# Optimization experiments

Hardware: AMD Instinct MI355X
Metric: run time of the kernel (lower is better)

The kernel has to match this reference:

```python
import jax, jax.numpy as jnp
import numpy as np

N = 10000
F_IN = 512
HID = 256
N_CLS = 64


def setup_inputs() -> dict:
    key = jax.random.key(0)
    k_feat, k_adj, k_w1, k_b1, k_w2, k_b2 = jax.random.split(key, 6)
    feature = jax.random.normal(k_feat, (N, F_IN), dtype=jnp.float32)
    # normalized-adjacency-like dense matrix (sparse-ish values, scaled)
    adj = jax.random.uniform(k_adj, (N, N), dtype=jnp.float32) * (1.0 / N)
    # GCNConv params: glorot-style weights, zero bias
    s1 = 1.0 / np.sqrt(F_IN)
    s2 = 1.0 / np.sqrt(HID)
    W1 = jax.random.uniform(k_w1, (F_IN, HID), jnp.float32, -s1, s1)
    b1 = jnp.zeros((HID,), jnp.float32)
    W2 = jax.random.uniform(k_w2, (HID, N_CLS), jnp.float32, -s2, s2)
    b2 = jnp.zeros((N_CLS,), jnp.float32)
    return {"feature": feature, "adj": adj, "W1": W1, "b1": b1, "W2": W2, "b2": b2}


def gcn_conv(x, adj, W, b):
    # support = x @ W ; out = adj @ support + b
    return adj @ (x @ W) + b


def reference(feature, adj, W1, b1, W2, b2):
    x1 = jax.nn.relu(gcn_conv(feature, adj, W1, b1))
    # dropout is identity in eval mode
    x2 = gcn_conv(x1, adj, W2, b2)
    return (x1, jax.nn.log_softmax(x2, axis=1))
```

## Files before the change

### kernel.cpp

```cpp
#include <hip/hip_runtime.h>
#include <hip/hip_bf16.h>


#define NROW 10000
#define FIN  512
#define HID  256
#define NCLS 64
#define KP   10048
#define KSPLIT2 4
#define KSPAN2  2560
#define KSPLIT4 8
#define KSPAN4  1280

typedef __bf16 bf8_t __attribute__((ext_vector_type(8)));
typedef __bf16 bf4_t __attribute__((ext_vector_type(4)));
typedef float  f4_t  __attribute__((ext_vector_type(4)));

typedef __attribute__((address_space(3))) void       lds_void;
typedef const __attribute__((address_space(1))) void glb_void;

__device__ __forceinline__ void dma16(const void* g, void* l) {
    __builtin_amdgcn_global_load_lds((glb_void*)g, (lds_void*)l, 16, 0, 0);
}

__device__ __forceinline__ int swzc(int k, int r) {
    return (k & ~63) | ((((k >> 3) & 7) ^ (r & 7)) << 3) | (k & 7);
}

template<int LDW>
__global__ void cvt_f32_bf16_swz(const float* __restrict__ in, __bf16* __restrict__ out, int n) {
    int stride = gridDim.x * blockDim.x * 4;
    for (int i = (blockIdx.x * blockDim.x + threadIdx.x) * 4; i < n; i += stride) {
        f4_t v = *(const f4_t*)(in + i);
        bf4_t o;
        o[0] = (__bf16)v[0]; o[1] = (__bf16)v[1]; o[2] = (__bf16)v[2]; o[3] = (__bf16)v[3];
        int row = i / LDW, k = i & (LDW - 1);
        *(bf4_t*)(out + (long)row * LDW + swzc(k, row)) = o;
    }
}

__global__ void cvt_transpose(const float* __restrict__ in, __bf16* __restrict__ out, int K, int Nn) {
    int idx = blockIdx.x * 256 + threadIdx.x;
    if (idx < K * Nn) {
        int k = idx / Nn, n = idx % Nn;
        out[(long)n * K + swzc(k, n)] = (__bf16)in[idx];
    }
}

template<int BN, bool AF32, int EPI>
__global__ void __launch_bounds__(256, (BN >= 128) ? 3 : 4)
gemm_bt(const void* __restrict__ Ap, const __bf16* __restrict__ Bt,
        int M, int Nn, int K, int Kclamp, int lda, int ldb, int kspan,
        float* __restrict__ outF, __bf16* __restrict__ outB,
        int ldo, long partStride)
{
    constexpr int BM = 64, BK = 64;
    constexpr int WM = BM / 2, WN = BN / 2;
    constexpr int MI = WM / 16, NI = WN / 16;
    constexpr int ACALLS = BM / 32;
    constexpr int BCALLS = BN / 32;
    constexpr int ASZ = BM * BK, BSZ = BN * BK;
    __shared__ __bf16 As[2 * ASZ];
    __shared__ __bf16 Bs[2 * BSZ];

    const int tid  = threadIdx.x;
    const int lane = tid & 63;
    const int wave = tid >> 6;
    const int wm = wave >> 1, wn = wave & 1;
    const int m0 = blockIdx.x * BM;
    const int n0 = blockIdx.y * BN;
    const int kbase = blockIdx.z * kspan;
    const int kend  = min(K, kbase + kspan);

    f4_t acc[MI][NI];
    #pragma unroll
    for (int i = 0; i < MI; i++)
        #pragma unroll
        for (int j = 0; j < NI; j++)
            acc[i][j] = f4_t{0.f, 0.f, 0.f, 0.f};

    const int lrow  = lane & 15;
    const int koff0 = (lane >> 4) * 8;
    const int l7    = lrow & 7;

    const __bf16* Brow[BCALLS];
    #pragma unroll
    for (int j = 0; j < BCALLS; ++j) {
        int c = wave + j * 4;
        Brow[j] = Bt + (long)(n0 + c * 8 + (lane >> 3)) * ldb + (lane & 7) * 8;
    }
    const __bf16* ArowB[ACALLS];
    const float*  ArowF[4];
    int Acol[4], AldsOff[4];
    if constexpr (AF32) {
        #pragma unroll
        for (int i = 0; i < 4; ++i) {
            int idx = tid + i * 256;
            int r = idx >> 4, c4 = idx & 15;
            ArowF[i] = (const float*)Ap + (long)min(m0 + r, M - 1) * lda;
            Acol[i] = c4 * 4;
            AldsOff[i] = r * BK + ((((c4 >> 1) ^ (r & 7)) << 3) | ((c4 & 1) * 4));
        }
    } else {
        #pragma unroll
        for (int j = 0; j < ACALLS; ++j) {
            int c = wave + j * 4;
            ArowB[j] = (const __bf16*)Ap + (long)(m0 + c * 8 + (lane >> 3)) * lda + (lane & 7) * 8;
        }
    }

    if constexpr (AF32) {
        f4_t av[4];
        #pragma unroll
        for (int i = 0; i < 4; ++i)
            av[i] = *(const f4_t*)(ArowF[i] + min(kbase + Acol[i], Kclamp - 4));
        #pragma unroll
        for (int i = 0; i < 4; ++i) {
            bf4_t o;
            o[0] = (__bf16)av[i][0]; o[1] = (__bf16)av[i][1];
            o[2] = (__bf16)av[i][2]; o[3] = (__bf16)av[i][3];
            *(bf4_t*)&As[AldsOff[i]] = o;
        }
    } else {
        #pragma unroll
        for (int j = 0; j < ACALLS; ++j)
            dma16(ArowB[j] + kbase, &As[(wave + j * 4) * 512]);
    }
    #pragma unroll
    for (int j = 0; j < BCALLS; ++j)
        dma16(Brow[j] + kbase, &Bs[(wave + j * 4) * 512]);
    __syncthreads();

    int cur = 0;
    for (int k0 = kbase; k0 < kend; k0 += BK) {
        const bool has_next = (k0 + BK < kend);
        const int nxt = cur ^ 1;
        f4_t av[4];
        if (has_next) {
            if constexpr (AF32) {
                #pragma unroll
                for (int i = 0; i < 4; ++i)
                    av[i] = *(const f4_t*)(ArowF[i] + min(k0 + BK + Acol[i], Kclamp - 4));
            } else {
                #pragma unroll
                for (int j = 0; j < ACALLS; ++j)
                    dma16(ArowB[j] + (k0 + BK), &As[nxt * ASZ + (wave + j * 4) * 512]);
            }
            #pragma unroll
            for (int j = 0; j < BCALLS; ++j)
                dma16(Brow[j] + (k0 + BK), &Bs[nxt * BSZ + (wave + j * 4) * 512]);
        }

        #pragma unroll
        for (int ks = 0; ks < BK; ks += 32) {
            const int cc = (ks + koff0) >> 3;
            const int co = ((cc ^ l7) << 3);
            bf8_t af[MI], bfv[NI];
            #pragma unroll
            for (int mi = 0; mi < MI; mi++)
                af[mi] = *(const bf8_t*)&As[cur * ASZ + (wm * WM + mi * 16 + lrow) * BK + co];
            #pragma unroll
            for (int ni = 0; ni < NI; ni++)
                bfv[ni] = *(const bf8_t*)&Bs[cur * BSZ + (wn * WN + ni * 16 + lrow) * BK + co];
            #pragma unroll
            for (int mi = 0; mi < MI; mi++)
                #pragma unroll
                for (int ni = 0; ni < NI; ni++)
                    acc[mi][ni] = __builtin_amdgcn_mfma_f32_16x16x32_bf16(
                        af[mi], bfv[ni], acc[mi][ni], 0, 0, 0);
        }

        if (has_next) {
            if constexpr (AF32) {
                #pragma unroll
                for (int i = 0; i < 4; ++i) {
                    bf4_t o;
                    o[0] = (__bf16)av[i][0]; o[1] = (__bf16)av[i][1];
                    o[2] = (__bf16)av[i][2]; o[3] = (__bf16)av[i][3];
                    *(bf4_t*)&As[nxt * ASZ + AldsOff[i]] = o;
                }
            }
        }
        __syncthreads();
        cur ^= 1;
    }

    const int erow = wm * WM + (lane >> 4) * 4;
    const int ecol = wn * WN + lrow;
    #pragma unroll
    for (int mi = 0; mi < MI; mi++) {
        #pragma unroll
        for (int ni = 0; ni < NI; ni++) {
            #pragma unroll
            for (int r = 0; r < 4; r++) {
                int grow = m0 + erow + mi * 16 + r;
                int gcol = n0 + ecol + ni * 16;
                if (grow < M && gcol < Nn) {
                    float v = acc[mi][ni][r];
                    if constexpr (EPI == 0) {
                        outB[(long)grow * ldo + swzc(gcol, grow)] = (__bf16)v;
                    } else {
                        outF[blockIdx.z * partStride + (long)grow * ldo + gcol] = v;
                    }
                }
            }
        }
    }
}

__global__ void relu_bias_fin(const float* __restrict__ part, const float* __restrict__ b1,
                              float* __restrict__ outF, __bf16* __restrict__ outB) {
    long i = (long)(blockIdx.x * 256 + threadIdx.x) * 4;
    f4_t v = *(const f4_t*)(part + i);
    #pragma unroll
    for (int s = 1; s < KSPLIT2; s++) {
        f4_t p = *(const f4_t*)(part + (long)s * NROW * HID + i);
        v[0] += p[0]; v[1] += p[1]; v[2] += p[2]; v[3] += p[3];
    }
    int row = (int)(i >> 8);
    int col = (int)(i & (HID - 1));
    f4_t b = *(const f4_t*)(b1 + col);
    f4_t y;
    bf4_t yb;
    #pragma unroll
    for (int j = 0; j < 4; j++) {
        y[j] = fmaxf(v[j] + b[j], 0.f);
        yb[j] = (__bf16)y[j];
    }
    *(f4_t*)(outF + i) = y;
    *(bf4_t*)(outB + (long)row * HID + swzc(col, row)) = yb;
}

__global__ void logsoftmax_fin(const float* __restrict__ part, const float* __restrict__ b2,
                               float* __restrict__ out, int M) {
    int row  = blockIdx.x * 4 + (threadIdx.x >> 6);
    int lane = threadIdx.x & 63;
    if (row >= M) return;
    float v = b2[lane];
    #pragma unroll
    for (int s = 0; s < KSPLIT4; s++) v += part[((long)s * M + row) * NCLS + lane];
    float m = v;
    #pragma unroll
    for (int off = 32; off > 0; off >>= 1) m = fmaxf(m, __shfl_xor(m, off));
    float e = __expf(v - m);
    float sum = e;
    #pragma unroll
    for (int off = 32; off > 0; off >>= 1) sum += __shfl_xor(sum, off);
    out[(long)row * NCLS + lane] = (v - m) - __logf(sum);
}

extern "C" void kernel_launch(void* const* d_in, const int* in_sizes, int n_in,
                              void* d_out, int out_size, void* d_ws, size_t ws_size,
                              hipStream_t stream) {
    const float* feat = (const float*)d_in[0];
    const float* adj  = (const float*)d_in[1];
    const float* W1   = (const float*)d_in[2];
    const float* b1   = (const float*)d_in[3];
    const float* W2   = (const float*)d_in[4];
    const float* b2   = (const float*)d_in[5];
    float* out = (float*)d_out;
    char* ws = (char*)d_ws;

    __bf16* featb = (__bf16*)(ws);
    __bf16* W1t   = (__bf16*)(ws + 10289152);
    __bf16* W2t   = (__bf16*)(ws + 10551296);
    __bf16* S1t   = (__bf16*)(ws + 10584064);
    __bf16* x1b   = (__bf16*)(ws + 15728640);
    __bf16* S2t   = (__bf16*)(ws + 20873216);
    float*  part  = (float*) (ws + 22159360);

    hipMemsetAsync(S1t, 0, (size_t)HID * KP * 2, stream);
    hipMemsetAsync(S2t, 0, (size_t)NCLS * KP * 2, stream);

    cvt_f32_bf16_swz<FIN><<<640, 256, 0, stream>>>(feat, featb, NROW * FIN);
    cvt_transpose<<<(FIN * HID + 255) / 256, 256, 0, stream>>>(W1, W1t, FIN, HID);
    cvt_transpose<<<(HID * NCLS + 255) / 256, 256, 0, stream>>>(W2, W2t, HID, NCLS);

    gemm_bt<64, false, 0><<<dim3(4, 157, 1), 256, 0, stream>>>(
        W1t, featb, HID, NROW, FIN, FIN, FIN, FIN, FIN,
        nullptr, S1t, KP, 0);

    gemm_bt<128, true, 2><<<dim3(157, 2, KSPLIT2), 256, 0, stream>>>(
        adj, S1t, NROW, HID, KP, NROW, NROW, KP, KSPAN2,
        part, nullptr, HID, (long)NROW * HID);

    relu_bias_fin<<<NROW * HID / 4 / 256, 256, 0, stream>>>(part, b1, out, x1b);

    gemm_bt<64, false, 0><<<dim3(1, 157, 1), 256, 0, stream>>>(
        W2t, x1b, NCLS, NROW, HID, HID, HID, HID, HID,
        nullptr, S2t, KP, 0);

    gemm_bt<64, true, 2><<<dim3(157, 1, KSPLIT4), 256, 0, stream>>>(
        adj, S2t, NROW, NCLS, KP, NROW, NROW, KP, KSPAN4,
        part, nullptr, NCLS, (long)NROW * NCLS);

    logsoftmax_fin<<<2500, 256, 0, stream>>>(part, b2, out + (long)NROW * HID, NROW);
}
```

Measured before the change: 737.5 us.

## Fuse conversion kernels, drop memsets, and halve split-K factors

Merges the three f32-to-bf16 conversion and transpose kernels into one launch, with block ranges that select which tensor each block converts. The two memsets that cleared the padded support buffers are removed; the support GEMM epilogue now writes zeros into the padding columns instead. The split-K factors for both adjacency GEMMs are halved, which reduces partial-sum traffic and reduction work. In exchange there are fewer blocks in flight per GEMM and longer K loops per block.

Result: slower. 753.2 us (+2.1%).

```diff
diff --git a/kernel.cpp b/kernel.cpp
--- a/kernel.cpp
+++ b/kernel.cpp
@@ -7,10 +7,10 @@
 #define HID  256
 #define NCLS 64
 #define KP   10048
-#define KSPLIT2 4
-#define KSPAN2  2560
-#define KSPLIT4 8
-#define KSPAN4  1280
+#define KSPLIT2 2
+#define KSPAN2  5056
+#define KSPLIT4 4
+#define KSPAN4  2560
 
 typedef __bf16 bf8_t __attribute__((ext_vector_type(8)));
 typedef __bf16 bf4_t __attribute__((ext_vector_type(4)));
@@ -27,23 +27,27 @@
     return (k & ~63) | ((((k >> 3) & 7) ^ (r & 7)) << 3) | (k & 7);
 }
 
-template<int LDW>
-__global__ void cvt_f32_bf16_swz(const float* __restrict__ in, __bf16* __restrict__ out, int n) {
-    int stride = gridDim.x * blockDim.x * 4;
-    for (int i = (blockIdx.x * blockDim.x + threadIdx.x) * 4; i < n; i += stride) {
-        f4_t v = *(const f4_t*)(in + i);
+#define FEAT_BLKS 5000
+#define W1_BLKS   512
+__global__ void cvt_all(const float* __restrict__ feat, const float* __restrict__ W1,
+                        const float* __restrict__ W2, __bf16* __restrict__ featb,
+                        __bf16* __restrict__ W1t, __bf16* __restrict__ W2t) {
+    int b = blockIdx.x;
+    if (b < FEAT_BLKS) {
+        int i = (b * 256 + threadIdx.x) * 4;
+        f4_t v = *(const f4_t*)(feat + i);
         bf4_t o;
         o[0] = (__bf16)v[0]; o[1] = (__bf16)v[1]; o[2] = (__bf16)v[2]; o[3] = (__bf16)v[3];
-        int row = i / LDW, k = i & (LDW - 1);
-        *(bf4_t*)(out + (long)row * LDW + swzc(k, row)) = o;
-    }
-}
-
-__global__ void cvt_transpose(const float* __restrict__ in, __bf16* __restrict__ out, int K, int Nn) {
-    int idx = blockIdx.x * 256 + threadIdx.x;
-    if (idx < K * Nn) {
-        int k = idx / Nn, n = idx % Nn;
-        out[(long)n * K + swzc(k, n)] = (__bf16)in[idx];
+        int row = i >> 9, k = i & (FIN - 1);
+        *(bf4_t*)(featb + (long)row * FIN + swzc(k, row)) = o;
+    } else if (b < FEAT_BLKS + W1_BLKS) {
+        int idx = (b - FEAT_BLKS) * 256 + threadIdx.x;
+        int k = idx / HID, n = idx % HID;
+        W1t[(long)n * FIN + swzc(k, n)] = (__bf16)W1[idx];
+    } else {
+        int idx = (b - FEAT_BLKS - W1_BLKS) * 256 + threadIdx.x;
+        int k = idx / NCLS, n = idx % NCLS;
+        W2t[(long)n * HID + swzc(k, n)] = (__bf16)W2[idx];
     }
 }
 
@@ -195,13 +199,14 @@
             for (int r = 0; r < 4; r++) {
                 int grow = m0 + erow + mi * 16 + r;
                 int gcol = n0 + ecol + ni * 16;
-                if (grow < M && gcol < Nn) {
-                    float v = acc[mi][ni][r];
-                    if constexpr (EPI == 0) {
+                if constexpr (EPI == 0) {
+                    if (grow < M) {
+                        float v = (gcol < Nn) ? acc[mi][ni][r] : 0.f;
                         outB[(long)grow * ldo + swzc(gcol, grow)] = (__bf16)v;
-                    } else {
-                        outF[blockIdx.z * partStride + (long)grow * ldo + gcol] = v;
                     }
+                } else {
+                    if (grow < M && gcol < Nn)
+                        outF[blockIdx.z * partStride + (long)grow * ldo + gcol] = acc[mi][ni][r];
                 }
             }
         }
@@ -269,12 +274,7 @@
     __bf16* S2t   = (__bf16*)(ws + 20873216);
     float*  part  = (float*) (ws + 22159360);
 
-    hipMemsetAsync(S1t, 0, (size_t)HID * KP * 2, stream);
-    hipMemsetAsync(S2t, 0, (size_t)NCLS * KP * 2, stream);
-
-    cvt_f32_bf16_swz<FIN><<<640, 256, 0, stream>>>(feat, featb, NROW * FIN);
-    cvt_transpose<<<(FIN * HID + 255) / 256, 256, 0, stream>>>(W1, W1t, FIN, HID);
-    cvt_transpose<<<(HID * NCLS + 255) / 256, 256, 0, stream>>>(W2, W2t, HID, NCLS);
+    cvt_all<<<FEAT_BLKS + W1_BLKS + 64, 256, 0, stream>>>(feat, W1, W2, featb, W1t, W2t);
 
     gemm_bt<64, false, 0><<<dim3(4, 157, 1), 256, 0, stream>>>(
         W1t, featb, HID, NROW, FIN, FIN, FIN, FIN, FIN,
```
